# Performance work log

Measured on AMD Instinct MI355X. Metric: run time of the kernel, lower is better.

## Reference

```python
import jax, jax.numpy as jnp
import numpy as np

N = 50000          # nodes
E = 1_600_000      # edges (avg degree 32)
IN = 16            # in_node_features
H0 = 64            # hidden_features_mlp[0]
D = 32             # hidden_features_mlp[1] == hidden_features_gnn
HF = 64            # hidden_final
OUT = 3            # out_features (congestion classes)
L = 3              # gnn_layer_num
EPS = 1e-5


def gelu(x):
    return jax.nn.gelu(x, approximate=False)  # torch nn.GELU default (erf)


def bn_eval(x, g, b):
    # BatchNorm1d in eval mode with fresh running stats (mean=0, var=1)
    return x * (g / jnp.sqrt(1.0 + EPS)) + b


def ln(x, g, b):
    m = jnp.mean(x, axis=-1, keepdims=True)
    v = jnp.var(x, axis=-1, keepdims=True)
    return (x - m) / jnp.sqrt(v + EPS) * g + b


def setup_inputs() -> dict:
    key = jax.random.key(0)
    ks = jax.random.split(key, 24)
    s = 0.1
    inp = {
        "x": jax.random.normal(ks[0], (N, IN), dtype=jnp.float32),
        "edge_index": jax.random.randint(ks[1], (2, E), 0, N, dtype=jnp.int32),
        # node_emb_mlp
        "emb_W1": jax.random.normal(ks[2], (IN, H0), dtype=jnp.float32) * s,
        "emb_b1": jnp.zeros((H0,), jnp.float32),
        "emb_bn1_g": jnp.ones((H0,), jnp.float32),
        "emb_bn1_b": jnp.zeros((H0,), jnp.float32),
        "emb_W2": jax.random.normal(ks[3], (H0, D), dtype=jnp.float32) * s,
        "emb_b2": jnp.zeros((D,), jnp.float32),
        "emb_bn2_g": jnp.ones((D,), jnp.float32),
        "emb_bn2_b": jnp.zeros((D,), jnp.float32),
        # GNN layers (stacked over L)
        "msg_W": jax.random.normal(ks[4], (L, 2 * D, D), dtype=jnp.float32) * s,
        "msg_b": jnp.zeros((L, D), jnp.float32),
        "msg_ln_g": jnp.ones((L, D), jnp.float32),
        "msg_ln_b": jnp.zeros((L, D), jnp.float32),
        "upd_W": jax.random.normal(ks[5], (L, 2 * D, D), dtype=jnp.float32) * s,
        "upd_b": jnp.zeros((L, D), jnp.float32),
        "upd_ln_g": jnp.ones((L, D), jnp.float32),
        "upd_ln_b": jnp.zeros((L, D), jnp.float32),
        # final_aggregation_layer
        "fin_W1": jax.random.normal(ks[6], (D, HF), dtype=jnp.float32) * s,
        "fin_b1": jnp.zeros((HF,), jnp.float32),
        "fin_bn_g": jnp.ones((HF,), jnp.float32),
        "fin_bn_b": jnp.zeros((HF,), jnp.float32),
        "fin_W2": jax.random.normal(ks[7], (HF, OUT), dtype=jnp.float32) * s,
        "fin_b2": jnp.zeros((OUT,), jnp.float32),
    }
    return inp


def reference(x, edge_index,
              emb_W1, emb_b1, emb_bn1_g, emb_bn1_b,
              emb_W2, emb_b2, emb_bn2_g, emb_bn2_b,
              msg_W, msg_b, msg_ln_g, msg_ln_b,
              upd_W, upd_b, upd_ln_g, upd_ln_b,
              fin_W1, fin_b1, fin_bn_g, fin_bn_b, fin_W2, fin_b2):
    src = edge_index[0]  # x_j (source, messages flow source->target)
    dst = edge_index[1]  # x_i (target, aggregation index)

    # node embedding MLP (dropout = identity in eval)
    h = gelu(bn_eval(x @ emb_W1 + emb_b1, emb_bn1_g, emb_bn1_b))
    h = gelu(bn_eval(h @ emb_W2 + emb_b2, emb_bn2_g, emb_bn2_b))
    pre = h

    for l in range(L):
        x_i = h[dst]  # [E, D]
        x_j = h[src]  # [E, D]
        m = gelu(ln(jnp.concatenate([x_i, x_j], axis=-1) @ msg_W[l] + msg_b[l],
                    msg_ln_g[l], msg_ln_b[l]))                 # [E, D]
        agg = jax.ops.segment_sum(m, dst, num_segments=N)      # [N, D]
        h = h + gelu(ln(jnp.concatenate([h, agg], axis=-1) @ upd_W[l] + upd_b[l],
                        upd_ln_g[l], upd_ln_b[l]))

    h = h + pre  # residual around the GNN stack

    general_emb = h[dst] - h[src]  # node_emb_j - node_emb_i, [E, D]
    out = gelu(bn_eval(general_emb @ fin_W1 + fin_b1, fin_bn_g, fin_bn_b))
    out = out @ fin_W2 + fin_b2  # [E, OUT] cc_scores
    return out
```

## Files before the change

### kernel.cpp

```cpp
#include <hip/hip_runtime.h>

#define NN 50000
#define NE 1600000
#define FILL_B 1563
#define EMB_B  782
#define HIST_STRIDE 100096
constexpr float LN_EPS = 1e-5f;

typedef _Float16 half8 __attribute__((ext_vector_type(8)));

__device__ __forceinline__ float gelu_f(float x){
  float ax = fabsf(x) * 0.70710678118654752440f;
  float t  = __builtin_amdgcn_rcpf(fmaf(0.3275911f, ax, 1.0f));
  float e  = __expf(-ax*ax);
  float p  = t*fmaf(t, fmaf(t, fmaf(t, fmaf(t, 1.061405429f, -1.453152027f),
                                    1.421413741f), -0.284496736f), 0.254829592f);
  float er = fmaf(-p, e, 1.0f);
  return 0.5f * x * (1.0f + copysignf(er, x));
}

__device__ __forceinline__ void ld8(const float* __restrict__ p, float* r){
  float4 a=((const float4*)p)[0], b=((const float4*)p)[1];
  r[0]=a.x;r[1]=a.y;r[2]=a.z;r[3]=a.w;r[4]=b.x;r[5]=b.y;r[6]=b.z;r[7]=b.w;
}
__device__ __forceinline__ void ld16(const float* __restrict__ p, float* r){ ld8(p,r); ld8(p+8,r+8); }
__device__ __forceinline__ void st8(float* __restrict__ p, const float* r){
  float4 a,b; a.x=r[0];a.y=r[1];a.z=r[2];a.w=r[3]; b.x=r[4];b.y=r[5];b.z=r[6];b.w=r[7];
  ((float4*)p)[0]=a; ((float4*)p)[1]=b;
}

__global__ __launch_bounds__(256) void hist_kernel(const int* __restrict__ ei,
    int* __restrict__ cnt8, int* __restrict__ rank){
  int t = blockIdx.x*256 + threadIdx.x;
  int hi = (blockIdx.x & 7) << 20;
  int* mycnt = cnt8 + (size_t)(blockIdx.x & 7)*NN;
  int i0 = t, i1 = t + HIST_STRIDE, i2 = t + 2*HIST_STRIDE, i3 = t + 3*HIST_STRIDE;
  bool v0 = i0 < NE/4, v1 = i1 < NE/4, v2 = i2 < NE/4, v3 = i3 < NE/4;
  int4 d0 = v0 ? ((const int4*)(ei + NE))[i0] : make_int4(0,0,0,0);
  int4 d1 = v1 ? ((const int4*)(ei + NE))[i1] : make_int4(0,0,0,0);
  int4 d2 = v2 ? ((const int4*)(ei + NE))[i2] : make_int4(0,0,0,0);
  int4 d3 = v3 ? ((const int4*)(ei + NE))[i3] : make_int4(0,0,0,0);
  int4 r0, r1, r2, r3;
  if(v0){ r0.x = hi|atomicAdd(&mycnt[d0.x],1); r0.y = hi|atomicAdd(&mycnt[d0.y],1);
          r0.z = hi|atomicAdd(&mycnt[d0.z],1); r0.w = hi|atomicAdd(&mycnt[d0.w],1); }
  if(v1){ r1.x = hi|atomicAdd(&mycnt[d1.x],1); r1.y = hi|atomicAdd(&mycnt[d1.y],1);
          r1.z = hi|atomicAdd(&mycnt[d1.z],1); r1.w = hi|atomicAdd(&mycnt[d1.w],1); }
  if(v2){ r2.x = hi|atomicAdd(&mycnt[d2.x],1); r2.y = hi|atomicAdd(&mycnt[d2.y],1);
          r2.z = hi|atomicAdd(&mycnt[d2.z],1); r2.w = hi|atomicAdd(&mycnt[d2.w],1); }
  if(v3){ r3.x = hi|atomicAdd(&mycnt[d3.x],1); r3.y = hi|atomicAdd(&mycnt[d3.y],1);
          r3.z = hi|atomicAdd(&mycnt[d3.z],1); r3.w = hi|atomicAdd(&mycnt[d3.w],1); }
  if(v0) ((int4*)rank)[i0] = r0;
  if(v1) ((int4*)rank)[i1] = r1;
  if(v2) ((int4*)rank)[i2] = r2;
  if(v3) ((int4*)rank)[i3] = r3;
}

__global__ __launch_bounds__(256) void reduce8_kernel(int* __restrict__ cnt8,
    int* __restrict__ deg){
  int t = blockIdx.x*256 + threadIdx.x;
  if(t >= NN/4) return;
  int4 c[8];
  #pragma unroll
  for(int x=0;x<8;x++) c[x] = ((const int4*)(cnt8 + (size_t)x*NN))[t];
  int4 run = make_int4(0,0,0,0);
  #pragma unroll
  for(int x=0;x<8;x++){
    ((int4*)(cnt8 + (size_t)x*NN))[t] = run;
    run.x += c[x].x; run.y += c[x].y; run.z += c[x].z; run.w += c[x].w;
  }
  ((int4*)deg)[t] = run;
}

#define CHUNK 52
__global__ __launch_bounds__(1024) void scan_kernel(const int* __restrict__ deg, int* __restrict__ row_ptr){
  __shared__ int sums[1024];
  int t = threadIdx.x;
  int base = t*CHUNK;
  int4 v[13];
  int ssum = 0;
  #pragma unroll
  for(int i=0;i<13;i++){
    int idx = base + 4*i;
    if(idx + 3 < NN){
      v[i] = ((const int4*)deg)[(base>>2)+i];
    } else {
      v[i].x = (idx+0<NN)?deg[idx+0]:0; v[i].y = (idx+1<NN)?deg[idx+1]:0;
      v[i].z = (idx+2<NN)?deg[idx+2]:0; v[i].w = (idx+3<NN)?deg[idx+3]:0;
    }
    ssum += v[i].x + v[i].y + v[i].z + v[i].w;
  }
  sums[t]=ssum;
  __syncthreads();
  for(int off=1; off<1024; off<<=1){
    int vv = (t>=off) ? sums[t-off] : 0;
    __syncthreads();
    sums[t] += vv;
    __syncthreads();
  }
  int run = (t>0) ? sums[t-1] : 0;
  #pragma unroll
  for(int i=0;i<13;i++){
    int idx = base + 4*i;
    int4 o;
    o.x = run; run += v[i].x;
    o.y = run; run += v[i].y;
    o.z = run; run += v[i].z;
    o.w = run; run += v[i].w;
    if(idx + 3 < NN){
      ((int4*)row_ptr)[(base>>2)+i] = o;
    } else {
      if(idx+0<NN) row_ptr[idx+0]=o.x;
      if(idx+1<NN) row_ptr[idx+1]=o.y;
      if(idx+2<NN) row_ptr[idx+2]=o.z;
      if(idx+3<NN) row_ptr[idx+3]=o.w;
    }
  }
  if(t==1023) row_ptr[NN] = sums[1023];
}

__global__ __launch_bounds__(256) void fill_embed_kernel(
    const int* __restrict__ ei, const int* __restrict__ row_ptr,
    const int* __restrict__ rank, const int* __restrict__ offs8,
    int* __restrict__ csr,
    const float* __restrict__ x,
    const float* __restrict__ W1, const float* __restrict__ b1,
    const float* __restrict__ g1, const float* __restrict__ bb1,
    const float* __restrict__ W2, const float* __restrict__ b2,
    const float* __restrict__ g2, const float* __restrict__ bb2,
    const float* __restrict__ Wm, const float* __restrict__ bm,
    const float* __restrict__ Wu, const float* __restrict__ bu,
    const float* __restrict__ fb1, const float* __restrict__ fbng, const float* __restrict__ fbnb,
    float* __restrict__ h, float* __restrict__ pre,
    float* __restrict__ P, _Float16* __restrict__ Qh, float* __restrict__ R,
    float* __restrict__ cvec)
{
  if(blockIdx.x >= EMB_B){
    int t = (blockIdx.x - EMB_B)*256 + threadIdx.x;
    if(t < NE/4){
      int4 d  = ((const int4*)(ei + NE))[t];
      int4 sv = ((const int4*)ei)[t];
      int4 rk = ((const int4*)rank)[t];
      csr[row_ptr[d.x] + offs8[(size_t)((unsigned)rk.x>>20)*NN + d.x] + (rk.x & 0xFFFFF)] = sv.x;
      csr[row_ptr[d.y] + offs8[(size_t)((unsigned)rk.y>>20)*NN + d.y] + (rk.y & 0xFFFFF)] = sv.y;
      csr[row_ptr[d.z] + offs8[(size_t)((unsigned)rk.z>>20)*NN + d.z] + (rk.z & 0xFFFFF)] = sv.z;
      csr[row_ptr[d.w] + offs8[(size_t)((unsigned)rk.w>>20)*NN + d.w] + (rk.w & 0xFFFFF)] = sv.w;
    }
    return;
  }
  int t = blockIdx.x*256 + threadIdx.x;
  const float rs = rsqrtf(1.0f + LN_EPS);
  if(t < 64) cvec[t] = fmaf(fb1[t], fbng[t]*rs, fbnb[t]);
  int n = t >> 2, q = t & 3;
  if(n >= NN) return;
  int base = threadIdx.x & 60;
  float4 xq = ((const float4*)x)[n*4 + q];
  float xv[16];
  #pragma unroll
  for(int m=0;m<4;m++){
    xv[4*m+0]=__shfl(xq.x, base|m);
    xv[4*m+1]=__shfl(xq.y, base|m);
    xv[4*m+2]=__shfl(xq.z, base|m);
    xv[4*m+3]=__shfl(xq.w, base|m);
  }
  float a1q[16]; ld16(b1 + q*16, a1q);
  #pragma unroll
  for(int k=0;k<16;k++){
    float w[16]; ld16(W1 + k*64 + q*16, w);
    float xk = xv[k];
    #pragma unroll
    for(int j=0;j<16;j++) a1q[j] += xk * w[j];
  }
  { float g[16], b[16]; ld16(g1+q*16,g); ld16(bb1+q*16,b);
    #pragma unroll
    for(int j=0;j<16;j++) a1q[j] = gelu_f(a1q[j]*(g[j]*rs) + b[j]); }
  float hq[8]; ld8(b2 + q*8, hq);
  #pragma unroll
  for(int m=0;m<4;m++){
    #pragma unroll
    for(int kk=0;kk<16;kk++){
      float a = __shfl(a1q[kk], base|m);
      float w[8]; ld8(W2 + (m*16+kk)*32 + q*8, w);
      #pragma unroll
      for(int j=0;j<8;j++) hq[j] += a * w[j];
    }
  }
  { float g[8], b[8]; ld8(g2+q*8,g); ld8(bb2+q*8,b);
    #pragma unroll
    for(int j=0;j<8;j++) hq[j] = gelu_f(hq[j]*(g[j]*rs) + b[j]); }
  st8(h   + (size_t)n*32 + q*8, hq);
  st8(pre + (size_t)n*32 + q*8, hq);
  float apv[8], aqv[8], arv[8];
  ld8(bm+q*8, apv); ld8(bu+q*8, arv);
  #pragma unroll
  for(int j=0;j<8;j++) aqv[j]=0.f;
  #pragma unroll
  for(int m=0;m<4;m++){
    #pragma unroll
    for(int kk=0;kk<8;kk++){
      float hk = __shfl(hq[kk], base|m);
      int k = m*8+kk;
      float wm[8],wq[8],wu[8];
      ld8(Wm + k*32      + q*8, wm);
      ld8(Wm + (32+k)*32 + q*8, wq);
      ld8(Wu + k*32      + q*8, wu);
      #pragma unroll
      for(int j=0;j<8;j++){ apv[j]+=hk*wm[j]; aqv[j]+=hk*wq[j]; arv[j]+=hk*wu[j]; }
    }
  }
  st8(P + (size_t)n*32 + q*8, apv);
  st8(R + (size_t)n*32 + q*8, arv);
  half8 qo;
  #pragma unroll
  for(int k=0;k<8;k++) qo[k] = (_Float16)aqv[k];
  *(half8*)(Qh + (size_t)n*32 + q*8) = qo;
}

__global__ __launch_bounds__(256) void msg_kernel(
    const float* __restrict__ P, const _Float16* __restrict__ Qh,
    const int* __restrict__ row_ptr, const int* __restrict__ csr_src,
    const float* __restrict__ mg, const float* __restrict__ mb,
    float* __restrict__ aggO)
{
  int tid = blockIdx.x*256 + threadIdx.x;
  int n = tid >> 4;
  int s = tid & 15;
  int slot = s >> 2;
  int q = s & 3;
  float mgq[8], mbq[8], p8[8];
  ld8(mg + q*8, mgq); ld8(mb + q*8, mbq);
  ld8(P + (size_t)n*32 + q*8, p8);
  float agg8[8] = {0,0,0,0,0,0,0,0};
  int e0 = row_ptr[n], e1 = row_ptr[n+1];
  int e = e0 + slot;
  int src = (e < e1) ? csr_src[e] : 0;
  half8 qv = *(const half8*)(Qh + (size_t)src*32 + q*8);
  while(e < e1){
    int e2 = e + 4;
    int src2 = (e2 < e1) ? csr_src[e2] : 0;
    half8 qv2 = *(const half8*)(Qh + (size_t)src2*32 + q*8);
    float v[8];
    #pragma unroll
    for(int k=0;k<8;k++) v[k] = p8[k] + (float)qv[k];
    float ps = ((v[0]+v[1])+(v[2]+v[3])) + ((v[4]+v[5])+(v[6]+v[7]));
    ps += __shfl_xor(ps,1); ps += __shfl_xor(ps,2);
    float mean = ps * 0.03125f;
    float vs = 0.f;
    #pragma unroll
    for(int k=0;k<8;k++){ float dd = v[k]-mean; vs += dd*dd; v[k]=dd; }
    vs += __shfl_xor(vs,1); vs += __shfl_xor(vs,2);
    float rstd = rsqrtf(vs*0.03125f + LN_EPS);
    #pragma unroll
    for(int k=0;k<8;k++) agg8[k] += gelu_f(v[k]*rstd*mgq[k] + mbq[k]);
    qv = qv2; e = e2;
  }
  #pragma unroll
  for(int k=0;k<8;k++) agg8[k] += __shfl_xor(agg8[k], 4);
  #pragma unroll
  for(int k=0;k<8;k++) agg8[k] += __shfl_xor(agg8[k], 8);
  if(slot==0) st8(aggO + (size_t)n*32 + q*8, agg8);
}

__global__ __launch_bounds__(256) void upd_pqr_kernel(
    const float* __restrict__ aggI, const float* __restrict__ Rio,
    const float* __restrict__ Ub,
    const float* __restrict__ ug, const float* __restrict__ ub,
    const float* __restrict__ Wm2, const float* __restrict__ bm2,
    const float* __restrict__ Wu2, const float* __restrict__ bu2,
    float* __restrict__ h,
    float* __restrict__ P, _Float16* __restrict__ Qh, float* __restrict__ Rout)
{
  int t = blockIdx.x*256 + threadIdx.x;
  int n = t >> 2, q = t & 3;
  if(n >= NN) return;
  int base = threadIdx.x & 60;
  float aggq[8], uq[8];
  ld8(aggI + (size_t)n*32 + q*8, aggq);
  ld8(Rio  + (size_t)n*32 + q*8, uq);
  #pragma unroll
  for(int m=0;m<4;m++){
    #pragma unroll
    for(int kk=0;kk<8;kk++){
      float a = __shfl(aggq[kk], base|m);
      float w[8]; ld8(Ub + (m*8+kk)*32 + q*8, w);
      #pragma unroll
      for(int j=0;j<8;j++) uq[j] += a * w[j];
    }
  }
  float sm = ((uq[0]+uq[1])+(uq[2]+uq[3])) + ((uq[4]+uq[5])+(uq[6]+uq[7]));
  sm += __shfl_xor(sm,1); sm += __shfl_xor(sm,2);
  float mean = sm * 0.03125f;
  float vs = 0.f;
  #pragma unroll
  for(int j=0;j<8;j++){ float d = uq[j]-mean; vs += d*d; uq[j]=d; }
  vs += __shfl_xor(vs,1); vs += __shfl_xor(vs,2);
  float rstd = rsqrtf(vs*0.03125f + LN_EPS);
  float ugq[8], ubq[8], hq[8];
  ld8(ug+q*8, ugq); ld8(ub+q*8, ubq);
  ld8(h + (size_t)n*32 + q*8, hq);
  #pragma unroll
  for(int j=0;j<8;j++) hq[j] += gelu_f(uq[j]*rstd*ugq[j] + ubq[j]);
  st8(h + (size_t)n*32 + q*8, hq);
  float apv[8], aqv[8], arv[8];
  ld8(bm2+q*8, apv); ld8(bu2+q*8, arv);
  #pragma unroll
  for(int j=0;j<8;j++) aqv[j]=0.f;
  #pragma unroll
  for(int m=0;m<4;m++){
    #pragma unroll
    for(int kk=0;kk<8;kk++){
      float hk = __shfl(hq[kk], base|m);
      int k = m*8+kk;
      float wm[8],wq[8],wu[8];
      ld8(Wm2 + k*32      + q*8, wm);
      ld8(Wm2 + (32+k)*32 + q*8, wq);
      ld8(Wu2 + k*32      + q*8, wu);
      #pragma unroll
      for(int j=0;j<8;j++){ apv[j]+=hk*wm[j]; aqv[j]+=hk*wq[j]; arv[j]+=hk*wu[j]; }
    }
  }
  st8(P    + (size_t)n*32 + q*8, apv);
  st8(Rout + (size_t)n*32 + q*8, arv);
  half8 qo;
  #pragma unroll
  for(int k=0;k<8;k++) qo[k] = (_Float16)aqv[k];
  *(half8*)(Qh + (size_t)n*32 + q*8) = qo;
}

__global__ __launch_bounds__(256) void upd_fin_kernel(
    const float* __restrict__ aggI, const float* __restrict__ Rio,
    const float* __restrict__ Ub,
    const float* __restrict__ ug, const float* __restrict__ ub,
    const float* __restrict__ h, const float* __restrict__ pre,
    const float* __restrict__ fW1, const float* __restrict__ fbng,
    _Float16* __restrict__ y1, _Float16* __restrict__ y2)
{
  int t = blockIdx.x*256 + threadIdx.x;
  int n = t >> 2, q = t & 3;
  if(n >= NN) return;
  int base = threadIdx.x & 60;
  const float rs = rsqrtf(1.0f + LN_EPS);
  float aggq[8], uq[8];
  ld8(aggI + (size_t)n*32 + q*8, aggq);
  ld8(Rio  + (size_t)n*32 + q*8, uq);
  #pragma unroll
  for(int m=0;m<4;m++){
    #pragma unroll
    for(int kk=0;kk<8;kk++){
      float a = __shfl(aggq[kk], base|m);
      float w[8]; ld8(Ub + (m*8+kk)*32 + q*8, w);
      #pragma unroll
      for(int j=0;j<8;j++) uq[j] += a * w[j];
    }
  }
  float sm = ((uq[0]+uq[1])+(uq[2]+uq[3])) + ((uq[4]+uq[5])+(uq[6]+uq[7]));
  sm += __shfl_xor(sm,1); sm += __shfl_xor(sm,2);
  float mean = sm * 0.03125f;
  float vs = 0.f;
  #pragma unroll
  for(int j=0;j<8;j++){ float d = uq[j]-mean; vs += d*d; uq[j]=d; }
  vs += __shfl_xor(vs,1); vs += __shfl_xor(vs,2);
  float rstd = rsqrtf(vs*0.03125f + LN_EPS);
  float ugq[8], ubq[8], hq[8], pq[8];
  ld8(ug+q*8, ugq); ld8(ub+q*8, ubq);
  ld8(h   + (size_t)n*32 + q*8, hq);
  ld8(pre + (size_t)n*32 + q*8, pq);
  #pragma unroll
  for(int j=0;j<8;j++) hq[j] += gelu_f(uq[j]*rstd*ugq[j] + ubq[j]) + pq[j];
  float acc[16];
  #pragma unroll
  for(int j=0;j<16;j++) acc[j]=0.f;
  #pragma unroll
  for(int m=0;m<4;m++){
    #pragma unroll
    for(int kk=0;kk<8;kk++){
      float hk = __shfl(hq[kk], base|m);
      float w[16]; ld16(fW1 + (m*8+kk)*64 + q*16, w);
      #pragma unroll
      for(int j=0;j<16;j++) acc[j] += hk * w[j];
    }
  }
  float fg[16]; ld16(fbng + q*16, fg);
  half8 o0, o1;
  #pragma unroll
  for(int k=0;k<8;k++){
    o0[k] = (_Float16)(acc[k]   * (fg[k]*rs));
    o1[k] = (_Float16)(acc[8+k] * (fg[8+k]*rs));
  }
  _Float16* dst = (q<2) ? (y1 + (size_t)n*32 + q*16) : (y2 + (size_t)n*32 + (q-2)*16);
  ((half8*)dst)[0] = o0; ((half8*)dst)[1] = o1;
}

__global__ __launch_bounds__(256) void finalA_kernel(
    const _Float16* __restrict__ y, const int* __restrict__ ei,
    const float* __restrict__ cvec, const float* __restrict__ W2,
    const float* __restrict__ b2, float* __restrict__ out)
{
  int t = blockIdx.x*256 + threadIdx.x;
  int e = t >> 2, q = t & 3;
  int s = __builtin_nontemporal_load(ei + e);
  int d = __builtin_nontemporal_load(ei + NE + e);
  half8 a8 = *(const half8*)(y + (size_t)d*32 + q*8);
  half8 c8 = *(const half8*)(y + (size_t)s*32 + q*8);
  float cq[8]; ld8(cvec + q*8, cq);
  float w[24]; ld8(W2+q*24, w); ld8(W2+q*24+8, w+8); ld8(W2+q*24+16, w+16);
  float o0=0.f,o1=0.f,o2=0.f;
  #pragma unroll
  for(int k=0;k<8;k++){
    float tt = gelu_f(((float)a8[k]-(float)c8[k]) + cq[k]);
    o0 += tt*w[3*k]; o1 += tt*w[3*k+1]; o2 += tt*w[3*k+2];
  }
  o0 += __shfl_xor(o0,1); o0 += __shfl_xor(o0,2);
  o1 += __shfl_xor(o1,1); o1 += __shfl_xor(o1,2);
  o2 += __shfl_xor(o2,1); o2 += __shfl_xor(o2,2);
  float ov = (q==0) ? o0 + b2[0] : (q==1) ? o1 + b2[1] : o2 + b2[2];
  if(q < 3) __builtin_nontemporal_store(ov, out + (size_t)e*3 + q);
}

__global__ __launch_bounds__(256) void finalB_kernel(
    const _Float16* __restrict__ y, const int* __restrict__ ei,
    const float* __restrict__ cvec, const float* __restrict__ W2,
    float* __restrict__ out)
{
  int t = blockIdx.x*256 + threadIdx.x;
  int e = t >> 2, q = t & 3;
  float prev = 0.f;
  if(q < 3) prev = __builtin_nontemporal_load(out + (size_t)e*3 + q);
  int s = __builtin_nontemporal_load(ei + e);
  int d = __builtin_nontemporal_load(ei + NE + e);
  half8 a8 = *(const half8*)(y + (size_t)d*32 + q*8);
  half8 c8 = *(const half8*)(y + (size_t)s*32 + q*8);
  float cq[8]; ld8(cvec + q*8, cq);
  float w[24]; ld8(W2+q*24, w); ld8(W2+q*24+8, w+8); ld8(W2+q*24+16, w+16);
  float o0=0.f,o1=0.f,o2=0.f;
  #pragma unroll
  for(int k=0;k<8;k++){
    float tt = gelu_f(((float)a8[k]-(float)c8[k]) + cq[k]);
    o0 += tt*w[3*k]; o1 += tt*w[3*k+1]; o2 += tt*w[3*k+2];
  }
  o0 += __shfl_xor(o0,1); o0 += __shfl_xor(o0,2);
  o1 += __shfl_xor(o1,1); o1 += __shfl_xor(o1,2);
  o2 += __shfl_xor(o2,1); o2 += __shfl_xor(o2,2);
  float ov = prev + ((q==0) ? o0 : (q==1) ? o1 : o2);
  if(q < 3) __builtin_nontemporal_store(ov, out + (size_t)e*3 + q);
}

extern "C" void kernel_launch(void* const* d_in, const int* in_sizes, int n_in,
                              void* d_out, int out_size, void* d_ws, size_t ws_size,
                              hipStream_t stream)
{
  (void)in_sizes; (void)n_in; (void)out_size; (void)ws_size;
  const float* x     = (const float*)d_in[0];
  const int*   ei    = (const int*)d_in[1];
  const float* eW1   = (const float*)d_in[2];
  const float* eb1   = (const float*)d_in[3];
  const float* ebn1g = (const float*)d_in[4];
  const float* ebn1b = (const float*)d_in[5];
  const float* eW2   = (const float*)d_in[6];
  const float* eb2   = (const float*)d_in[7];
  const float* ebn2g = (const float*)d_in[8];
  const float* ebn2b = (const float*)d_in[9];
  const float* msgW  = (const float*)d_in[10];
  const float* msgb  = (const float*)d_in[11];
  const float* msglng= (const float*)d_in[12];
  const float* msglnb= (const float*)d_in[13];
  const float* updW  = (const float*)d_in[14];
  const float* updb  = (const float*)d_in[15];
  const float* updlng= (const float*)d_in[16];
  const float* updlnb= (const float*)d_in[17];
  const float* fW1   = (const float*)d_in[18];
  const float* fb1   = (const float*)d_in[19];
  const float* fbng  = (const float*)d_in[20];
  const float* fbnb  = (const float*)d_in[21];
  const float* fW2   = (const float*)d_in[22];
  const float* fb2   = (const float*)d_in[23];
  float* out = (float*)d_out;

  float* f   = (float*)d_ws;
  float* h   = f;
  float* pre = f + 1*(size_t)NN*32;
  float* P   = f + 2*(size_t)NN*32;
  float* R   = f + 3*(size_t)NN*32;
  float* agg = f + 4*(size_t)NN*32;
  _Float16* Qh = (_Float16*)(f + 5*(size_t)NN*32);
  _Float16* y1 = (_Float16*)P;
  _Float16* y2 = y1 + (size_t)NN*32;
  float* cvec  = f + 5*(size_t)NN*32 + (size_t)NN*16;
  int* ip      = (int*)(cvec + 64);
  int* cnt8    = ip;
  int* deg     = ip + 8*NN;
  int* row_ptr = ip + 9*NN;
  int* csr     = ip + 10*NN + 4;
  int* rank    = (int*)agg;

  hipMemsetAsync(cnt8, 0, (size_t)8*NN*sizeof(int), stream);
  hist_kernel<<<391, 256, 0, stream>>>(ei, cnt8, rank);
  reduce8_kernel<<<(NN/4+255)/256, 256, 0, stream>>>(cnt8, deg);
  scan_kernel<<<1, 1024, 0, stream>>>(deg, row_ptr);
  fill_embed_kernel<<<EMB_B + FILL_B, 256, 0, stream>>>(ei, row_ptr, rank, cnt8, csr,
      x, eW1, eb1, ebn1g, ebn1b,
      eW2, eb2, ebn2g, ebn2b,
      msgW, msgb, updW, updb,
      fb1, fbng, fbnb,
      h, pre, P, Qh, R, cvec);

  for(int l=0; l<3; l++){
    msg_kernel<<<(NN*16)/256, 256, 0, stream>>>(P, Qh, row_ptr, csr,
        msglng + l*32, msglnb + l*32, agg);
    if(l < 2){
      upd_pqr_kernel<<<EMB_B, 256, 0, stream>>>(agg, R,
          updW + l*2048 + 1024, updlng + l*32, updlnb + l*32,
          msgW + (l+1)*2048, msgb + (l+1)*32,
          updW + (l+1)*2048, updb + (l+1)*32,
          h, P, Qh, R);
    } else {
      upd_fin_kernel<<<EMB_B, 256, 0, stream>>>(agg, R,
          updW + l*2048 + 1024, updlng + l*32, updlnb + l*32,
          h, pre, fW1, fbng, y1, y2);
    }
  }

  finalA_kernel<<<(NE*4)/256, 256, 0, stream>>>(y1, ei, cvec,      fW2,      fb2, out);
  finalB_kernel<<<(NE*4)/256, 256, 0, stream>>>(y2, ei, cvec + 32, fW2 + 96, out);
}
```

Baseline: 500.6 us.

## Widen histogram copies, use 8 edge slots per node, two edges per final thread

The histogram now spreads atomics over 16 per-block-group count copies instead of 8, which is meant to cut atomic contention at the cost of a larger memset and reduce pass. The message kernel gives each node 32 lanes (8 edge slots) instead of 16, adding one more shuffle-reduction step. This shortens per-node serial loops but spends more lanes on low-degree nodes. The final edge kernels each process two edges per thread, halving the grid and raising memory-level parallelism per thread at the cost of more registers.

```diff
diff --git a/kernel.cpp b/kernel.cpp
--- a/kernel.cpp
+++ b/kernel.cpp
@@ -30,10 +30,10 @@
 }
 
 __global__ __launch_bounds__(256) void hist_kernel(const int* __restrict__ ei,
-    int* __restrict__ cnt8, int* __restrict__ rank){
-  int t = blockIdx.x*256 + threadIdx.x;
-  int hi = (blockIdx.x & 7) << 20;
-  int* mycnt = cnt8 + (size_t)(blockIdx.x & 7)*NN;
+    int* __restrict__ cnt16, int* __restrict__ rank){
+  int t = blockIdx.x*256 + threadIdx.x;
+  int hi = (blockIdx.x & 15) << 20;
+  int* mycnt = cnt16 + (size_t)(blockIdx.x & 15)*NN;
   int i0 = t, i1 = t + HIST_STRIDE, i2 = t + 2*HIST_STRIDE, i3 = t + 3*HIST_STRIDE;
   bool v0 = i0 < NE/4, v1 = i1 < NE/4, v2 = i2 < NE/4, v3 = i3 < NE/4;
   int4 d0 = v0 ? ((const int4*)(ei + NE))[i0] : make_int4(0,0,0,0);
@@ -55,18 +55,16 @@
   if(v3) ((int4*)rank)[i3] = r3;
 }
 
-__global__ __launch_bounds__(256) void reduce8_kernel(int* __restrict__ cnt8,
+__global__ __launch_bounds__(256) void reduce16_kernel(int* __restrict__ cnt16,
     int* __restrict__ deg){
   int t = blockIdx.x*256 + threadIdx.x;
   if(t >= NN/4) return;
-  int4 c[8];
-  #pragma unroll
-  for(int x=0;x<8;x++) c[x] = ((const int4*)(cnt8 + (size_t)x*NN))[t];
   int4 run = make_int4(0,0,0,0);
   #pragma unroll
-  for(int x=0;x<8;x++){
-    ((int4*)(cnt8 + (size_t)x*NN))[t] = run;
-    run.x += c[x].x; run.y += c[x].y; run.z += c[x].z; run.w += c[x].w;
+  for(int x=0;x<16;x++){
+    int4 c = ((const int4*)(cnt16 + (size_t)x*NN))[t];
+    ((int4*)(cnt16 + (size_t)x*NN))[t] = run;
+    run.x += c.x; run.y += c.y; run.z += c.z; run.w += c.w;
   }
   ((int4*)deg)[t] = run;
 }
@@ -120,7 +118,7 @@
 
 __global__ __launch_bounds__(256) void fill_embed_kernel(
     const int* __restrict__ ei, const int* __restrict__ row_ptr,
-    const int* __restrict__ rank, const int* __restrict__ offs8,
+    const int* __restrict__ rank, const int* __restrict__ offs16,
     int* __restrict__ csr,
     const float* __restrict__ x,
     const float* __restrict__ W1, const float* __restrict__ b1,
@@ -140,10 +138,10 @@
       int4 d  = ((const int4*)(ei + NE))[t];
       int4 sv = ((const int4*)ei)[t];
       int4 rk = ((const int4*)rank)[t];
-      csr[row_ptr[d.x] + offs8[(size_t)((unsigned)rk.x>>20)*NN + d.x] + (rk.x & 0xFFFFF)] = sv.x;
-      csr[row_ptr[d.y] + offs8[(size_t)((unsigned)rk.y>>20)*NN + d.y] + (rk.y & 0xFFFFF)] = sv.y;
-      csr[row_ptr[d.z] + offs8[(size_t)((unsigned)rk.z>>20)*NN + d.z] + (rk.z & 0xFFFFF)] = sv.z;
-      csr[row_ptr[d.w] + offs8[(size_t)((unsigned)rk.w>>20)*NN + d.w] + (rk.w & 0xFFFFF)] = sv.w;
+      csr[row_ptr[d.x] + offs16[(size_t)((unsigned)rk.x>>20)*NN + d.x] + (rk.x & 0xFFFFF)] = sv.x;
+      csr[row_ptr[d.y] + offs16[(size_t)((unsigned)rk.y>>20)*NN + d.y] + (rk.y & 0xFFFFF)] = sv.y;
+      csr[row_ptr[d.z] + offs16[(size_t)((unsigned)rk.z>>20)*NN + d.z] + (rk.z & 0xFFFFF)] = sv.z;
+      csr[row_ptr[d.w] + offs16[(size_t)((unsigned)rk.w>>20)*NN + d.w] + (rk.w & 0xFFFFF)] = sv.w;
     }
     return;
   }
@@ -222,8 +220,8 @@
     float* __restrict__ aggO)
 {
   int tid = blockIdx.x*256 + threadIdx.x;
-  int n = tid >> 4;
-  int s = tid & 15;
+  int n = tid >> 5;
+  int s = tid & 31;
   int slot = s >> 2;
   int q = s & 3;
   float mgq[8], mbq[8], p8[8];
@@ -235,7 +233,7 @@
   int src = (e < e1) ? csr_src[e] : 0;
   half8 qv = *(const half8*)(Qh + (size_t)src*32 + q*8);
   while(e < e1){
-    int e2 = e + 4;
+    int e2 = e + 8;
     int src2 = (e2 < e1) ? csr_src[e2] : 0;
     half8 qv2 = *(const half8*)(Qh + (size_t)src2*32 + q*8);
     float v[8];
@@ -257,6 +255,8 @@
   for(int k=0;k<8;k++) agg8[k] += __shfl_xor(agg8[k], 4);
   #pragma unroll
   for(int k=0;k<8;k++) agg8[k] += __shfl_xor(agg8[k], 8);
+  #pragma unroll
+  for(int k=0;k<8;k++) agg8[k] += __shfl_xor(agg8[k], 16);
   if(slot==0) st8(aggO + (size_t)n*32 + q*8, agg8);
 }
 
@@ -396,24 +396,38 @@
     const float* __restrict__ b2, float* __restrict__ out)
 {
   int t = blockIdx.x*256 + threadIdx.x;
-  int e = t >> 2, q = t & 3;
-  int s = __builtin_nontemporal_load(ei + e);
-  int d = __builtin_nontemporal_load(ei + NE + e);
-  half8 a8 = *(const half8*)(y + (size_t)d*32 + q*8);
-  half8 c8 = *(const half8*)(y + (size_t)s*32 + q*8);
+  int g = t >> 2, q = t & 3;
+  int eA = g, eB = g + NE/2;
+  int sA = __builtin_nontemporal_load(ei + eA);
+  int dA = __builtin_nontemporal_load(ei + NE + eA);
+  int sB = __builtin_nontemporal_load(ei + eB);
+  int dB = __builtin_nontemporal_load(ei + NE + eB);
+  half8 aA = *(const half8*)(y + (size_t)dA*32 + q*8);
+  half8 cA = *(const half8*)(y + (size_t)sA*32 + q*8);
+  half8 aB = *(const half8*)(y + (size_t)dB*32 + q*8);
+  half8 cB = *(const half8*)(y + (size_t)sB*32 + q*8);
   float cq[8]; ld8(cvec + q*8, cq);
   float w[24]; ld8(W2+q*24, w); ld8(W2+q*24+8, w+8); ld8(W2+q*24+16, w+16);
-  float o0=0.f,o1=0.f,o2=0.f;
+  float oA0=0.f,oA1=0.f,oA2=0.f, oB0=0.f,oB1=0.f,oB2=0.f;
   #pragma unroll
   for(int k=0;k<8;k++){
-    float tt = gelu_f(((float)a8[k]-(float)c8[k]) + cq[k]);
-    o0 += tt*w[3*k]; o1 += tt*w[3*k+1]; o2 += tt*w[3*k+2];
-  }
-  o0 += __shfl_xor(o0,1); o0 += __shfl_xor(o0,2);
-  o1 += __shfl_xor(o1,1); o1 += __shfl_xor(o1,2);
-  o2 += __shfl_xor(o2,1); o2 += __shfl_xor(o2,2);
-  float ov = (q==0) ? o0 + b2[0] : (q==1) ? o1 + b2[1] : o2 + b2[2];
-  if(q < 3) __builtin_nontemporal_store(ov, out + (size_t)e*3 + q);
+    float tA = gelu_f(((float)aA[k]-(float)cA[k]) + cq[k]);
+    float tB = gelu_f(((float)aB[k]-(float)cB[k]) + cq[k]);
+    oA0 += tA*w[3*k]; oA1 += tA*w[3*k+1]; oA2 += tA*w[3*k+2];
+    oB0 += tB*w[3*k]; oB1 += tB*w[3*k+1]; oB2 += tB*w[3*k+2];
+  }
+  oA0 += __shfl_xor(oA0,1); oA0 += __shfl_xor(oA0,2);
+  oA1 += __shfl_xor(oA1,1); oA1 += __shfl_xor(oA1,2);
+  oA2 += __shfl_xor(oA2,1); oA2 += __shfl_xor(oA2,2);
+  oB0 += __shfl_xor(oB0,1); oB0 += __shfl_xor(oB0,2);
+  oB1 += __shfl_xor(oB1,1); oB1 += __shfl_xor(oB1,2);
+  oB2 += __shfl_xor(oB2,1); oB2 += __shfl_xor(oB2,2);
+  float ovA = (q==0) ? oA0 + b2[0] : (q==1) ? oA1 + b2[1] : oA2 + b2[2];
+  float ovB = (q==0) ? oB0 + b2[0] : (q==1) ? oB1 + b2[1] : oB2 + b2[2];
+  if(q < 3){
+    __builtin_nontemporal_store(ovA, out + (size_t)eA*3 + q);
+    __builtin_nontemporal_store(ovB, out + (size_t)eB*3 + q);
+  }
 }
 
 __global__ __launch_bounds__(256) void finalB_kernel(
@@ -422,26 +436,43 @@
     float* __restrict__ out)
 {
   int t = blockIdx.x*256 + threadIdx.x;
-  int e = t >> 2, q = t & 3;
-  float prev = 0.f;
-  if(q < 3) prev = __builtin_nontemporal_load(out + (size_t)e*3 + q);
-  int s = __builtin_nontemporal_load(ei + e);
-  int d = __builtin_nontemporal_load(ei + NE + e);
-  half8 a8 = *(const half8*)(y + (size_t)d*32 + q*8);
-  half8 c8 = *(const half8*)(y + (size_t)s*32 + q*8);
+  int g = t >> 2, q = t & 3;
+  int eA = g, eB = g + NE/2;
+  float pA = 0.f, pB = 0.f;
+  if(q < 3){
+    pA = __builtin_nontemporal_load(out + (size_t)eA*3 + q);
+    pB = __builtin_nontemporal_load(out + (size_t)eB*3 + q);
+  }
+  int sA = __builtin_nontemporal_load(ei + eA);
+  int dA = __builtin_nontemporal_load(ei + NE + eA);
+  int sB = __builtin_nontemporal_load(ei + eB);
+  int dB = __builtin_nontemporal_load(ei + NE + eB);
+  half8 aA = *(const half8*)(y + (size_t)dA*32 + q*8);
+  half8 cA = *(const half8*)(y + (size_t)sA*32 + q*8);
+  half8 aB = *(const half8*)(y + (size_t)dB*32 + q*8);
+  half8 cB = *(const half8*)(y + (size_t)sB*32 + q*8);
   float cq[8]; ld8(cvec + q*8, cq);
   float w[24]; ld8(W2+q*24, w); ld8(W2+q*24+8, w+8); ld8(W2+q*24+16, w+16);
-  float o0=0.f,o1=0.f,o2=0.f;
+  float oA0=0.f,oA1=0.f,oA2=0.f, oB0=0.f,oB1=0.f,oB2=0.f;
   #pragma unroll
   for(int k=0;k<8;k++){
-    float tt = gelu_f(((float)a8[k]-(float)c8[k]) + cq[k]);
-    o0 += tt*w[3*k]; o1 += tt*w[3*k+1]; o2 += tt*w[3*k+2];
-  }
-  o0 += __shfl_xor(o0,1); o0 += __shfl_xor(o0,2);
-  o1 += __shfl_xor(o1,1); o1 += __shfl_xor(o1,2);
-  o2 += __shfl_xor(o2,1); o2 += __shfl_xor(o2,2);
-  float ov = prev + ((q==0) ? o0 : (q==1) ? o1 : o2);
-  if(q < 3) __builtin_nontemporal_store(ov, out + (size_t)e*3 + q);
+    float tA = gelu_f(((float)aA[k]-(float)cA[k]) + cq[k]);
+    float tB = gelu_f(((float)aB[k]-(float)cB[k]) + cq[k]);
+    oA0 += tA*w[3*k]; oA1 += tA*w[3*k+1]; oA2 += tA*w[3*k+2];
+    oB0 += tB*w[3*k]; oB1 += tB*w[3*k+1]; oB2 += tB*w[3*k+2];
+  }
+  oA0 += __shfl_xor(oA0,1); oA0 += __shfl_xor(oA0,2);
+  oA1 += __shfl_xor(oA1,1); oA1 += __shfl_xor(oA1,2);
+  oA2 += __shfl_xor(oA2,1); oA2 += __shfl_xor(oA2,2);
+  oB0 += __shfl_xor(oB0,1); oB0 += __shfl_xor(oB0,2);
+  oB1 += __shfl_xor(oB1,1); oB1 += __shfl_xor(oB1,2);
+  oB2 += __shfl_xor(oB2,1); oB2 += __shfl_xor(oB2,2);
+  float ovA = pA + ((q==0) ? oA0 : (q==1) ? oA1 : oA2);
+  float ovB = pB + ((q==0) ? oB0 : (q==1) ? oB1 : oB2);
+  if(q < 3){
+    __builtin_nontemporal_store(ovA, out + (size_t)eA*3 + q);
+    __builtin_nontemporal_store(ovB, out + (size_t)eB*3 + q);
+  }
 }
 
 extern "C" void kernel_launch(void* const* d_in, const int* in_sizes, int n_in,
@@ -486,17 +517,17 @@
   _Float16* y2 = y1 + (size_t)NN*32;
   float* cvec  = f + 5*(size_t)NN*32 + (size_t)NN*16;
   int* ip      = (int*)(cvec + 64);
-  int* cnt8    = ip;
-  int* deg     = ip + 8*NN;
-  int* row_ptr = ip + 9*NN;
-  int* csr     = ip + 10*NN + 4;
+  int* cnt16   = ip;
+  int* deg     = ip + 16*NN;
+  int* row_ptr = ip + 17*NN;
+  int* csr     = ip + 18*NN + 4;
   int* rank    = (int*)agg;
 
-  hipMemsetAsync(cnt8, 0, (size_t)8*NN*sizeof(int), stream);
-  hist_kernel<<<391, 256, 0, stream>>>(ei, cnt8, rank);
-  reduce8_kernel<<<(NN/4+255)/256, 256, 0, stream>>>(cnt8, deg);
+  hipMemsetAsync(cnt16, 0, (size_t)16*NN*sizeof(int), stream);
+  hist_kernel<<<391, 256, 0, stream>>>(ei, cnt16, rank);
+  reduce16_kernel<<<(NN/4+255)/256, 256, 0, stream>>>(cnt16, deg);
   scan_kernel<<<1, 1024, 0, stream>>>(deg, row_ptr);
-  fill_embed_kernel<<<EMB_B + FILL_B, 256, 0, stream>>>(ei, row_ptr, rank, cnt8, csr,
+  fill_embed_kernel<<<EMB_B + FILL_B, 256, 0, stream>>>(ei, row_ptr, rank, cnt16, csr,
       x, eW1, eb1, ebn1g, ebn1b,
       eW2, eb2, ebn2g, ebn2b,
       msgW, msgb, updW, updb,
@@ -504,7 +535,7 @@
       h, pre, P, Qh, R, cvec);
 
   for(int l=0; l<3; l++){
-    msg_kernel<<<(NN*16)/256, 256, 0, stream>>>(P, Qh, row_ptr, csr,
+    msg_kernel<<<(NN*32)/256, 256, 0, stream>>>(P, Qh, row_ptr, csr,
         msglng + l*32, msglnb + l*32, agg);
     if(l < 2){
       upd_pqr_kernel<<<EMB_B, 256, 0, stream>>>(agg, R,
@@ -519,6 +550,6 @@
     }
   }
 
-  finalA_kernel<<<(NE*4)/256, 256, 0, stream>>>(y1, ei, cvec,      fW2,      fb2, out);
-  finalB_kernel<<<(NE*4)/256, 256, 0, stream>>>(y2, ei, cvec + 32, fW2 + 96, out);
-}
+  finalA_kernel<<<(NE*2)/256, 256, 0, stream>>>(y1, ei, cvec,      fW2,      fb2, out);
+  finalB_kernel<<<(NE*2)/256, 256, 0, stream>>>(y2, ei, cvec + 32, fW2 + 96, out);
+}
```

New measurement: 488.9 us. 2.3% less time.
